# Optimization experiments

Measured on AMD Instinct MI355X. Metric: run time of the kernel, lower is better.

The kernel has to match this reference:

```python
import jax, jax.numpy as jnp
import numpy as np

H = 128          # hidden_dim
N_LAYERS = 3
N_GRAPHS = 256
LN_EPS = 1e-5


def setup_inputs() -> dict:
    key = jax.random.key(0)
    ks = jax.random.split(key, 12)
    N, E = 100000, 600000
    x = jax.random.normal(ks[0], (N, 66), dtype=jnp.float32)
    edge_index = jax.random.randint(ks[1], (2, E), 0, N, dtype=jnp.int32)
    edge_attr = jax.random.normal(ks[2], (E, 6), dtype=jnp.float32)
    batch = jnp.sort(jax.random.randint(ks[3], (N,), 0, N_GRAPHS, dtype=jnp.int32))
    # params (stored as [in, out] so y = x @ W + b)
    def lin(k, fan_in, fan_out):
        s = 1.0 / np.sqrt(fan_in)
        kw, kb = jax.random.split(k)
        return (jax.random.uniform(kw, (fan_in, fan_out), jnp.float32, -s, s),
                jax.random.uniform(kb, (fan_out,), jnp.float32, -s, s))
    w_node, b_node = lin(ks[4], 66, H)
    w_edge, b_edge = lin(ks[5], 6, H)
    mp_ws, mp_bs = [], []
    for i in range(N_LAYERS):
        w, b = lin(ks[6 + i], 3 * H, H)
        mp_ws.append(w); mp_bs.append(b)
    w_out, b_out = lin(ks[9], H, H)
    return {
        "x": x, "edge_index": edge_index, "edge_attr": edge_attr, "batch": batch,
        "w_node": w_node, "b_node": b_node, "w_edge": w_edge, "b_edge": b_edge,
        "mp_w": jnp.stack(mp_ws), "mp_b": jnp.stack(mp_bs),
        "ln_g": jnp.ones((H,), jnp.float32), "ln_b": jnp.zeros((H,), jnp.float32),
        "w_out": w_out, "b_out": b_out,
    }


def _layer_norm(h, g, b):
    mu = h.mean(-1, keepdims=True)
    var = ((h - mu) ** 2).mean(-1, keepdims=True)
    return (h - mu) * jax.lax.rsqrt(var + LN_EPS) * g + b


def reference(x, edge_index, edge_attr, batch, w_node, b_node, w_edge, b_edge,
              mp_w, mp_b, ln_g, ln_b, w_out, b_out):
    h = x @ w_node + b_node                      # [N, H]
    ef = edge_attr @ w_edge + b_edge             # [E, H]
    src, dst = edge_index[0], edge_index[1]
    for i in range(N_LAYERS):
        W = mp_w[i]                               # [3H, H], split to avoid concat
        Ws, Wd, We = W[:H], W[H:2 * H], W[2 * H:]
        # per-edge message = Linear(concat(h[src], h[dst], ef)); original takes a
        # GLOBAL mean over all edges -> single [H] vector broadcast to all nodes
        msgs = h[src] @ Ws + h[dst] @ Wd + ef @ We   # [E, H]
        mean_msg = msgs.mean(axis=0) + mp_b[i]       # [H]
        h = h + mean_msg
        h = jax.nn.relu(_layer_norm(h, ln_g, ln_b))
        # dropout is identity in eval mode
    counts = jax.ops.segment_sum(jnp.ones((h.shape[0],), h.dtype), batch,
                                 num_segments=N_GRAPHS)
    pooled = jax.ops.segment_sum(h, batch, num_segments=N_GRAPHS)
    pooled = pooled / jnp.maximum(counts, 1.0)[:, None]   # global_mean_pool
    return pooled @ w_out + b_out                 # [N_GRAPHS, H]
```

## Files before the change

### kernel.cpp

```cpp
#include <hip/hip_runtime.h>

#define HDIM 128
#define XDIM 66
#define EDIM 6
#define NGRAPHS 256
#define LN_EPS 1e-5f

#define NWORDS 25600
#define CBINS 102400
#define HB 64
#define NBX 1024
#define KP 104
#define NES 16

typedef __attribute__((ext_vector_type(8))) short sv8;
typedef __attribute__((ext_vector_type(4))) float fv4;

__device__ __forceinline__ unsigned short f2bf(float f) {
    unsigned u = __float_as_uint(f);
    return (unsigned short)((u + 0x7FFFu + ((u >> 16) & 1u)) >> 16);
}
__device__ __forceinline__ float bf2f(unsigned short u) {
    return __uint_as_float((unsigned)u << 16);
}

__global__ __launch_bounds__(1024) void k_hist(const int* __restrict__ ei,
        unsigned* __restrict__ part, int E) {
    __shared__ unsigned lh[NWORDS];
    int b = blockIdx.x;
    int s = b & (HB - 1);
    int a = b / HB;
    int t = threadIdx.x;
    for (int i = t; i < NWORDS; i += 1024) lh[i] = 0u;
    __syncthreads();
    const int* src = ei + (size_t)a * E;
    int chunk = (((E + HB - 1) / HB) + 3) & ~3;
    int lo = s * chunk;
    int hi = min(E, lo + chunk);
    if ((E & 3) == 0) {
        for (int i = lo + t * 4; i + 4 <= hi; i += 1024 * 4) {
            int4 v = *(const int4*)(src + i);
            atomicAdd(&lh[v.x >> 2], 1u << ((v.x & 3) * 8));
            atomicAdd(&lh[v.y >> 2], 1u << ((v.y & 3) * 8));
            atomicAdd(&lh[v.z >> 2], 1u << ((v.z & 3) * 8));
            atomicAdd(&lh[v.w >> 2], 1u << ((v.w & 3) * 8));
        }
    } else {
        for (int i = lo + t; i < hi; i += 1024) {
            int v = src[i];
            atomicAdd(&lh[v >> 2], 1u << ((v & 3) * 8));
        }
    }
    __syncthreads();
    unsigned* dst = part + (size_t)b * NWORDS;
    for (int i = t; i < NWORDS / 4; i += 1024)
        ((uint4*)dst)[i] = ((const uint4*)lh)[i];
}

__global__ __launch_bounds__(256) void k_hist_red(const unsigned* __restrict__ part,
        float* __restrict__ c_src, float* __restrict__ c_dst) {
    int w = blockIdx.x * 256 + threadIdx.x;
    if (w >= NWORDS) return;
    unsigned a0 = 0, a1 = 0;
    const unsigned* p0 = part + w;
    const unsigned* p1 = part + (size_t)HB * NWORDS + w;
#pragma unroll 8
    for (int s = 0; s < HB; ++s) {
        a0 += p0[(size_t)s * NWORDS];
        a1 += p1[(size_t)s * NWORDS];
    }
    float4 o0, o1;
    o0.x = (float)(a0 & 0xFF);         o0.y = (float)((a0 >> 8) & 0xFF);
    o0.z = (float)((a0 >> 16) & 0xFF); o0.w = (float)(a0 >> 24);
    o1.x = (float)(a1 & 0xFF);         o1.y = (float)((a1 >> 8) & 0xFF);
    o1.z = (float)((a1 >> 16) & 0xFF); o1.w = (float)(a1 >> 24);
    *(float4*)(c_src + 4 * w) = o0;
    *(float4*)(c_dst + 4 * w) = o1;
}

__global__ __launch_bounds__(256) void k_misc(const float* __restrict__ ea,
        float* __restrict__ sum_attr, int E, const float* __restrict__ w_node,
        unsigned short* __restrict__ wtg) {
    int b = blockIdx.x;
    int t = threadIdx.x;
    if (b < NES) {
        int nchunk = E >> 1;
        float a0 = 0, a1 = 0, a2 = 0, a3 = 0, a4 = 0, a5 = 0;
        for (int c = b * 256 + t; c < nchunk; c += NES * 256) {
            const float4* p = (const float4*)(ea + (size_t)c * 12);
            float4 v0 = p[0], v1 = p[1], v2 = p[2];
            a0 += v0.x + v1.z;  a1 += v0.y + v1.w;  a2 += v0.z + v2.x;
            a3 += v0.w + v2.y;  a4 += v1.x + v2.z;  a5 += v1.y + v2.w;
        }
#pragma unroll
        for (int m = 32; m; m >>= 1) {
            a0 += __shfl_xor(a0, m); a1 += __shfl_xor(a1, m); a2 += __shfl_xor(a2, m);
            a3 += __shfl_xor(a3, m); a4 += __shfl_xor(a4, m); a5 += __shfl_xor(a5, m);
        }
        __shared__ float sb[4][6];
        int lane = t & 63, w = t >> 6;
        if (lane == 0) {
            sb[w][0] = a0; sb[w][1] = a1; sb[w][2] = a2;
            sb[w][3] = a3; sb[w][4] = a4; sb[w][5] = a5;
        }
        __syncthreads();
        if (t < 6) {
            float s = sb[0][t] + sb[1][t] + sb[2][t] + sb[3][t];
            atomicAdd(&sum_attr[t], s);
        }
        if (b == 0 && t < 6 && (E & 1))
            atomicAdd(&sum_attr[t], ea[(size_t)(E - 1) * 6 + t]);
    } else {
        if (t < 128) {
            for (int kp = 0; kp < KP; ++kp) {
                float v = (kp < XDIM) ? w_node[kp * HDIM + t] : 0.f;
                wtg[t * KP + kp] = f2bf(v);
            }
        }
    }
}

__global__ __launch_bounds__(256) void k_xsum(const float* __restrict__ x,
        const float* __restrict__ c_src, const float* __restrict__ c_dst,
        float* __restrict__ xpart, int N) {
    int lane = threadIdx.x & 63, w = threadIdx.x >> 6;
    int wid = blockIdx.x * 4 + w, nw = gridDim.x * 4;
    float as0 = 0, ad0 = 0, as1 = 0, ad1 = 0;
    int Q = N >> 2;
    for (int q = wid; q < Q; q += nw) {
        int n = q * 4;
        const float* xr = x + (size_t)n * XDIM;
        float x0 = xr[lane];
        float x1 = xr[XDIM + lane];
        float x2 = xr[2 * XDIM + lane];
        float x3 = xr[3 * XDIM + lane];
        float4 cs = *(const float4*)(c_src + n);
        float4 cd = *(const float4*)(c_dst + n);
        as0 = fmaf(cs.x, x0, as0); as0 = fmaf(cs.y, x1, as0);
        as0 = fmaf(cs.z, x2, as0); as0 = fmaf(cs.w, x3, as0);
        ad0 = fmaf(cd.x, x0, ad0); ad0 = fmaf(cd.y, x1, ad0);
        ad0 = fmaf(cd.z, x2, ad0); ad0 = fmaf(cd.w, x3, ad0);
        if (lane < 2) {
            float e0 = xr[64 + lane];
            float e1 = xr[XDIM + 64 + lane];
            float e2 = xr[2 * XDIM + 64 + lane];
            float e3 = xr[3 * XDIM + 64 + lane];
            as1 = fmaf(cs.x, e0, as1); as1 = fmaf(cs.y, e1, as1);
            as1 = fmaf(cs.z, e2, as1); as1 = fmaf(cs.w, e3, as1);
            ad1 = fmaf(cd.x, e0, ad1); ad1 = fmaf(cd.y, e1, ad1);
            ad1 = fmaf(cd.z, e2, ad1); ad1 = fmaf(cd.w, e3, ad1);
        }
    }
    if (wid == 0) {
        for (int n = Q * 4; n < N; ++n) {
            const float* xr = x + (size_t)n * XDIM;
            float cs = c_src[n], cd = c_dst[n];
            float xv = xr[lane];
            as0 = fmaf(cs, xv, as0);
            ad0 = fmaf(cd, xv, ad0);
            if (lane < 2) {
                float xe = xr[64 + lane];
                as1 = fmaf(cs, xe, as1);
                ad1 = fmaf(cd, xe, ad1);
            }
        }
    }
    __shared__ float redS[4][XDIM], redD[4][XDIM];
    redS[w][lane] = as0;  redD[w][lane] = ad0;
    if (lane < 2) { redS[w][64 + lane] = as1;  redD[w][64 + lane] = ad1; }
    __syncthreads();
    int t = threadIdx.x;
    float* xp = xpart + (size_t)blockIdx.x * 136;
    if (t < XDIM) {
        xp[t]        = redS[0][t] + redS[1][t] + redS[2][t] + redS[3][t];
        xp[XDIM + t] = redD[0][t] + redD[1][t] + redD[2][t] + redD[3][t];
    }
}

__global__ __launch_bounds__(64) void k_xred(const float* __restrict__ xpart,
                                             float* __restrict__ xs, int nb) {
    int e = blockIdx.x;
    int lane = threadIdx.x;
    float s = 0.f;
    for (int b = lane; b < nb; b += 64)
        s += xpart[(size_t)b * 136 + e];
#pragma unroll
    for (int m = 32; m; m >>= 1) s += __shfl_xor(s, m);
    if (lane == 0) xs[e] = s;
}

__global__ __launch_bounds__(256) void k_red(const float* __restrict__ partials,
                                             float* __restrict__ sbuf, int nb) {
    int b0 = blockIdx.x * 32;
    int b1 = min(nb, b0 + 32);
    int t = threadIdx.x;
    float s0 = 0.f, s1 = 0.f;
    for (int b = b0; b < b1; ++b) {
        const float* row = partials + (size_t)b * 512;
        s0 += row[t];
        s1 += row[t + 256];
    }
    atomicAdd(&sbuf[t], s0);
    atomicAdd(&sbuf[t + 256], s1);
}

template <int FIRST>
__global__ __launch_bounds__(256) void k_mm(const float* __restrict__ sv,
        const float* __restrict__ sum_attr, const float* __restrict__ w_edge,
        const float* __restrict__ b_edge, const float* __restrict__ W,
        const float* __restrict__ mpb, float* __restrict__ mean_msg, float Ef,
        const float* __restrict__ w_node, const float* __restrict__ b_node) {
    __shared__ float sc[384];
    __shared__ float mred[256];
    int t = threadIdx.x;
    if (t < 128) {
        float ssrc, sdst;
        if (FIRST) {
            ssrc = Ef * b_node[t];
            sdst = ssrc;
#pragma unroll
            for (int k = 0; k < XDIM; ++k) {
                float wv = w_node[k * HDIM + t];
                ssrc = fmaf(sv[k], wv, ssrc);
                sdst = fmaf(sv[XDIM + k], wv, sdst);
            }
        } else {
            ssrc = sv[t] + sv[t + 128];
            sdst = sv[256 + t] + sv[384 + t];
        }
        sc[t] = ssrc;
        sc[128 + t] = sdst;
        float se = Ef * b_edge[t];
#pragma unroll
        for (int k = 0; k < EDIM; ++k) se = fmaf(sum_attr[k], w_edge[k * HDIM + t], se);
        sc[256 + t] = se;
    }
    __syncthreads();
    int col = blockIdx.x * 16 + (t & 15);
    int rg = t >> 4;
    float acc = 0.f;
#pragma unroll 4
    for (int r = rg * 24; r < rg * 24 + 24; ++r)
        acc = fmaf(sc[r], W[r * HDIM + col], acc);
    mred[t] = acc;
    __syncthreads();
    if (t < 16) {
        float s = 0.f;
#pragma unroll
        for (int g = 0; g < 16; ++g) s += mred[g * 16 + t];
        mean_msg[blockIdx.x * 16 + t] = s / Ef + mpb[blockIdx.x * 16 + t];
    }
}

__global__ __launch_bounds__(256) void k_upd0(
        const float* __restrict__ x, const unsigned short* __restrict__ wtg,
        const float* __restrict__ b_node, const float* __restrict__ mean_msg,
        const float* __restrict__ ln_g, const float* __restrict__ ln_b,
        const float* __restrict__ c_src, const float* __restrict__ c_dst,
        unsigned short* __restrict__ h, float* __restrict__ partials, int N) {
    __shared__ unsigned short xl[64 * KP];
    __shared__ unsigned short wt[128 * KP];
    int t = threadIdx.x;
    int lane = t & 63, w = t >> 6;
    {
        const uint4* srcp = (const uint4*)wtg;
        uint4* dstp = (uint4*)wt;
        for (int i = t; i < 128 * KP / 8; i += 256) dstp[i] = srcp[i];
    }
    for (int i = t; i < 64 * KP / 2; i += 256) ((unsigned*)xl)[i] = 0u;
    __syncthreads();
    int rowbase = blockIdx.x * 64;
    const float* xg = x + (size_t)rowbase * XDIM;
    int lim = min(64, N - rowbase) * XDIM;
    for (int i = t; i < 64 * XDIM; i += 256) {
        if (i < lim) {
            int r = i / XDIM, k = i - r * XDIM;
            xl[r * KP + k] = f2bf(xg[i]);
        }
    }
    int cl = lane & 15, g = lane >> 4;
    float bm[8], gg[8], lb[8];
#pragma unroll
    for (int ct = 0; ct < 8; ++ct) {
        int col = ct * 16 + cl;
        bm[ct] = b_node[col] + mean_msg[col];
        gg[ct] = ln_g[col];
        lb[ct] = ln_b[col];
    }
    __syncthreads();

    fv4 acc[8];
#pragma unroll
    for (int ct = 0; ct < 8; ++ct) acc[ct] = (fv4){0.f, 0.f, 0.f, 0.f};
#pragma unroll
    for (int ks = 0; ks < 3; ++ks) {
        sv8 a = *(const sv8*)&xl[(w * 16 + cl) * KP + ks * 32 + g * 8];
#pragma unroll
        for (int ct = 0; ct < 8; ++ct) {
            sv8 b = *(const sv8*)&wt[(ct * 16 + cl) * KP + ks * 32 + g * 8];
            acc[ct] = __builtin_amdgcn_mfma_f32_16x16x32_bf16(a, b, acc[ct], 0, 0, 0);
        }
    }
    float v[8][4];
    float s[4] = {0.f, 0.f, 0.f, 0.f};
#pragma unroll
    for (int ct = 0; ct < 8; ++ct)
#pragma unroll
        for (int e = 0; e < 4; ++e) {
            v[ct][e] = acc[ct][e] + bm[ct];
            s[e] += v[ct][e];
        }
#pragma unroll
    for (int m = 1; m < 16; m <<= 1) {
        s[0] += __shfl_xor(s[0], m); s[1] += __shfl_xor(s[1], m);
        s[2] += __shfl_xor(s[2], m); s[3] += __shfl_xor(s[3], m);
    }
    float mu[4], q[4] = {0.f, 0.f, 0.f, 0.f};
#pragma unroll
    for (int e = 0; e < 4; ++e) mu[e] = s[e] * (1.0f / HDIM);
#pragma unroll
    for (int ct = 0; ct < 8; ++ct)
#pragma unroll
        for (int e = 0; e < 4; ++e) {
            float d = v[ct][e] - mu[e];
            q[e] = fmaf(d, d, q[e]);
        }
#pragma unroll
    for (int m = 1; m < 16; m <<= 1) {
        q[0] += __shfl_xor(q[0], m); q[1] += __shfl_xor(q[1], m);
        q[2] += __shfl_xor(q[2], m); q[3] += __shfl_xor(q[3], m);
    }
    float rs[4];
#pragma unroll
    for (int e = 0; e < 4; ++e) rs[e] = rsqrtf(q[e] * (1.0f / HDIM) + LN_EPS);

    int grow = rowbase + w * 16 + g * 4;
    float4 csv = *(const float4*)(c_src + grow);
    float4 cdv = *(const float4*)(c_dst + grow);
    float cs[4] = {csv.x, csv.y, csv.z, csv.w};
    float cd[4] = {cdv.x, cdv.y, cdv.z, cdv.w};
    float accS[8], accD[8];
#pragma unroll
    for (int ct = 0; ct < 8; ++ct) { accS[ct] = 0.f; accD[ct] = 0.f; }
#pragma unroll
    for (int e = 0; e < 4; ++e) {
        int row = grow + e;
        bool ok = (row < N);
#pragma unroll
        for (int ct = 0; ct < 8; ++ct) {
            float o = fmaxf(0.f, fmaf((v[ct][e] - mu[e]) * rs[e], gg[ct], lb[ct]));
            if (ok) h[(size_t)row * HDIM + ct * 16 + cl] = f2bf(o);
            accS[ct] = fmaf(cs[e], o, accS[ct]);
            accD[ct] = fmaf(cd[e], o, accD[ct]);
        }
    }
#pragma unroll
    for (int ct = 0; ct < 8; ++ct) {
        accS[ct] += __shfl_xor(accS[ct], 16); accS[ct] += __shfl_xor(accS[ct], 32);
        accD[ct] += __shfl_xor(accD[ct], 16); accD[ct] += __shfl_xor(accD[ct], 32);
    }
    __syncthreads();
    float* redS = (float*)xl;
    float* redD = redS + 512;
    if (g == 0) {
#pragma unroll
        for (int ct = 0; ct < 8; ++ct) {
            redS[w * HDIM + ct * 16 + cl] = accS[ct];
            redD[w * HDIM + ct * 16 + cl] = accD[ct];
        }
    }
    __syncthreads();
    if (t < 128) {
        float ss = redS[t] + redS[128 + t] + redS[256 + t] + redS[384 + t];
        float dd = redD[t] + redD[128 + t] + redD[256 + t] + redD[384 + t];
        float* row = partials + (size_t)blockIdx.x * 512;
        row[t] = ss;       row[t + 128] = 0.f;
        row[t + 256] = dd; row[t + 384] = 0.f;
    }
}

__device__ __forceinline__ float4 ln_row4(const unsigned short* hp,
        float4 mm, float4 g, float4 bb) {
    ushort4 hv = *(const ushort4*)hp;
    float4 v;
    v.x = bf2f(hv.x) + mm.x; v.y = bf2f(hv.y) + mm.y;
    v.z = bf2f(hv.z) + mm.z; v.w = bf2f(hv.w) + mm.w;
    float s = v.x + v.y + v.z + v.w;
#pragma unroll
    for (int m = 1; m < 32; m <<= 1) s += __shfl_xor(s, m);
    float mu = s * (1.0f / HDIM);
    float d0 = v.x - mu, d1 = v.y - mu, d2 = v.z - mu, d3 = v.w - mu;
    float q = d0 * d0 + d1 * d1 + d2 * d2 + d3 * d3;
#pragma unroll
    for (int m = 1; m < 32; m <<= 1) q += __shfl_xor(q, m);
    float rs = rsqrtf(q * (1.0f / HDIM) + LN_EPS);
    float4 o;
    o.x = fmaxf(0.f, fmaf(d0 * rs, g.x, bb.x));
    o.y = fmaxf(0.f, fmaf(d1 * rs, g.y, bb.y));
    o.z = fmaxf(0.f, fmaf(d2 * rs, g.z, bb.z));
    o.w = fmaxf(0.f, fmaf(d3 * rs, g.w, bb.w));
    return o;
}

template <int LAST>
__global__ __launch_bounds__(256) void k_update(
        unsigned short* __restrict__ h, const float* __restrict__ mean_msg,
        const float* __restrict__ ln_g, const float* __restrict__ ln_b,
        const float* __restrict__ c_src, const float* __restrict__ c_dst,
        const int* __restrict__ batch, float* __restrict__ partials,
        float* __restrict__ pooled, int N, int cpb) {
    int t = threadIdx.x;
    int lane = t & 63, w = t >> 6;
    int half = lane >> 5, cl = lane & 31;
    int c0 = cl * 4;
    float4 mm = *(const float4*)(mean_msg + c0);
    float4 g  = *(const float4*)(ln_g + c0);
    float4 bb = *(const float4*)(ln_b + c0);
    int start = blockIdx.x * cpb;
    int end = min(N, start + cpb);
    int spw = (cpb + 3) >> 2;
    int ns = start + w * spw;
    int ne = min(end, ns + spw);
    float4 accS = {0,0,0,0}, accD = {0,0,0,0}, accP = {0,0,0,0};
    int cur_g = -1;
    int n = ns;
    for (; n + 4 <= ne; n += 4) {
        int rA = n + half, rB = n + 2 + half;
        float4 oA = ln_row4(h + (size_t)rA * HDIM + c0, mm, g, bb);
        float4 oB = ln_row4(h + (size_t)rB * HDIM + c0, mm, g, bb);
        if (LAST) {
            int gA = batch[rA], gB = batch[rB];
            if (gA != cur_g) {
                if (cur_g >= 0) {
                    atomicAdd(&pooled[cur_g * HDIM + c0],     accP.x);
                    atomicAdd(&pooled[cur_g * HDIM + c0 + 1], accP.y);
                    atomicAdd(&pooled[cur_g * HDIM + c0 + 2], accP.z);
                    atomicAdd(&pooled[cur_g * HDIM + c0 + 3], accP.w);
                }
                accP = (float4){0,0,0,0};
                cur_g = gA;
            }
            accP.x += oA.x; accP.y += oA.y; accP.z += oA.z; accP.w += oA.w;
            if (gB != cur_g) {
                if (cur_g >= 0) {
                    atomicAdd(&pooled[cur_g * HDIM + c0],     accP.x);
                    atomicAdd(&pooled[cur_g * HDIM + c0 + 1], accP.y);
                    atomicAdd(&pooled[cur_g * HDIM + c0 + 2], accP.z);
                    atomicAdd(&pooled[cur_g * HDIM + c0 + 3], accP.w);
                }
                accP = (float4){0,0,0,0};
                cur_g = gB;
            }
            accP.x += oB.x; accP.y += oB.y; accP.z += oB.z; accP.w += oB.w;
        } else {
            ushort4 pA = {f2bf(oA.x), f2bf(oA.y), f2bf(oA.z), f2bf(oA.w)};
            ushort4 pB = {f2bf(oB.x), f2bf(oB.y), f2bf(oB.z), f2bf(oB.w)};
            *(ushort4*)(h + (size_t)rA * HDIM + c0) = pA;
            *(ushort4*)(h + (size_t)rB * HDIM + c0) = pB;
            float csA = c_src[rA], cdA = c_dst[rA];
            float csB = c_src[rB], cdB = c_dst[rB];
            accS.x = fmaf(csA, oA.x, accS.x); accS.y = fmaf(csA, oA.y, accS.y);
            accS.z = fmaf(csA, oA.z, accS.z); accS.w = fmaf(csA, oA.w, accS.w);
            accS.x = fmaf(csB, oB.x, accS.x); accS.y = fmaf(csB, oB.y, accS.y);
            accS.z = fmaf(csB, oB.z, accS.z); accS.w = fmaf(csB, oB.w, accS.w);
            accD.x = fmaf(cdA, oA.x, accD.x); accD.y = fmaf(cdA, oA.y, accD.y);
            accD.z = fmaf(cdA, oA.z, accD.z); accD.w = fmaf(cdA, oA.w, accD.w);
            accD.x = fmaf(cdB, oB.x, accD.x); accD.y = fmaf(cdB, oB.y, accD.y);
            accD.z = fmaf(cdB, oB.z, accD.z); accD.w = fmaf(cdB, oB.w, accD.w);
        }
    }
    for (; n < ne; n += 2) {
        int row = n + half;
        bool ok = row < ne;
        int rsafe = ok ? row : (N - 1);
        float4 o = ln_row4(h + (size_t)rsafe * HDIM + c0, mm, g, bb);
        if (LAST) {
            if (ok) {
                int gg2 = batch[row];
                if (gg2 != cur_g) {
                    if (cur_g >= 0) {
                        atomicAdd(&pooled[cur_g * HDIM + c0],     accP.x);
                        atomicAdd(&pooled[cur_g * HDIM + c0 + 1], accP.y);
                        atomicAdd(&pooled[cur_g * HDIM + c0 + 2], accP.z);
                        atomicAdd(&pooled[cur_g * HDIM + c0 + 3], accP.w);
                    }
                    accP = (float4){0,0,0,0};
                    cur_g = gg2;
                }
                accP.x += o.x; accP.y += o.y; accP.z += o.z; accP.w += o.w;
            }
        } else if (ok) {
            ushort4 pk = {f2bf(o.x), f2bf(o.y), f2bf(o.z), f2bf(o.w)};
            *(ushort4*)(h + (size_t)row * HDIM + c0) = pk;
            float cs = c_src[row], cd = c_dst[row];
            accS.x = fmaf(cs, o.x, accS.x); accS.y = fmaf(cs, o.y, accS.y);
            accS.z = fmaf(cs, o.z, accS.z); accS.w = fmaf(cs, o.w, accS.w);
            accD.x = fmaf(cd, o.x, accD.x); accD.y = fmaf(cd, o.y, accD.y);
            accD.z = fmaf(cd, o.z, accD.z); accD.w = fmaf(cd, o.w, accD.w);
        }
    }
    if (LAST) {
        if (cur_g >= 0) {
            atomicAdd(&pooled[cur_g * HDIM + c0],     accP.x);
            atomicAdd(&pooled[cur_g * HDIM + c0 + 1], accP.y);
            atomicAdd(&pooled[cur_g * HDIM + c0 + 2], accP.z);
            atomicAdd(&pooled[cur_g * HDIM + c0 + 3], accP.w);
        }
    } else {
        __shared__ float redS[8][HDIM], redD[8][HDIM];
        int set = (w << 1) | half;
        *(float4*)(&redS[set][c0]) = accS;
        *(float4*)(&redD[set][c0]) = accD;
        __syncthreads();
        if (t < 128) {
            float ss = 0.f, dd = 0.f;
#pragma unroll
            for (int gi = 0; gi < 8; ++gi) {
                ss += redS[gi][t];
                dd += redD[gi][t];
            }
            float* row = partials + (size_t)blockIdx.x * 512;
            row[t] = ss;       row[t + 128] = 0.f;
            row[t + 256] = dd; row[t + 384] = 0.f;
        }
    }
}

__global__ __launch_bounds__(128) void k_out(const float* __restrict__ pooled,
        const int* __restrict__ batch, const float* __restrict__ w_out,
        const float* __restrict__ b_out, float* __restrict__ out, int N) {
    int gph = blockIdx.x;
    int t = threadIdx.x;
    __shared__ float p[HDIM];
    __shared__ int cntS;
    if (t == 0) {
        int lo = 0, hi = N;
        while (lo < hi) { int mid = (lo + hi) >> 1; if (batch[mid] < gph) lo = mid + 1; else hi = mid; }
        int lo2 = lo, hi2 = N;
        while (lo2 < hi2) { int mid = (lo2 + hi2) >> 1; if (batch[mid] <= gph) lo2 = mid + 1; else hi2 = mid; }
        cntS = lo2 - lo;
    }
    __syncthreads();
    float inv = 1.0f / fmaxf((float)cntS, 1.0f);
    p[t] = pooled[gph * HDIM + t] * inv;
    __syncthreads();
    float acc = b_out[t];
#pragma unroll 8
    for (int k = 0; k < HDIM; ++k) acc = fmaf(p[k], w_out[k * HDIM + t], acc);
    out[gph * HDIM + t] = acc;
}

extern "C" void kernel_launch(void* const* d_in, const int* in_sizes, int n_in,
                              void* d_out, int out_size, void* d_ws, size_t ws_size,
                              hipStream_t stream) {
    const float* x      = (const float*)d_in[0];
    const int*   ei     = (const int*)d_in[1];
    const float* ea     = (const float*)d_in[2];
    const int*   batch  = (const int*)d_in[3];
    const float* w_node = (const float*)d_in[4];
    const float* b_node = (const float*)d_in[5];
    const float* w_edge = (const float*)d_in[6];
    const float* b_edge = (const float*)d_in[7];
    const float* mp_w   = (const float*)d_in[8];
    const float* mp_b   = (const float*)d_in[9];
    const float* ln_g   = (const float*)d_in[10];
    const float* ln_b   = (const float*)d_in[11];
    const float* w_out  = (const float*)d_in[12];
    const float* b_out  = (const float*)d_in[13];
    float* out = (float*)d_out;
    int N = in_sizes[3];
    int E = in_sizes[2] / EDIM;
    float Ef = (float)E;
    int ntiles0 = (N + 63) / 64;

    float* ws = (float*)d_ws;
    size_t off = 0;
    unsigned short* h = (unsigned short*)(ws + off);
    unsigned* hist_part = (unsigned*)(ws + off);
    off += (size_t)N * HDIM / 2;
    float* partials = ws + off; off += (size_t)2048 * 512;
    float* mean_msg = ws + off; off += 128;
    float* c_src    = ws + off; off += CBINS;
    float* c_dst    = ws + off; off += CBINS;
    float* xpart    = ws + off; off += (size_t)NBX * 136;
    unsigned short* wtg = (unsigned short*)(ws + off); off += 128 * KP / 2;
    float* xs       = ws + off; off += 136;
    float* acc0     = ws + off;
    float* sum_attr = ws + off; off += 8;
    float* sbuf1    = ws + off; off += 512;
    float* sbuf2    = ws + off; off += 512;
    float* pooled   = ws + off; off += NGRAPHS * HDIM;
    size_t zero_count = (size_t)(ws + off - acc0);
    hipMemsetAsync(acc0, 0, zero_count * sizeof(float), stream);

    k_misc<<<NES + 1, 256, 0, stream>>>(ea, sum_attr, E, w_node, wtg);
    k_hist<<<2 * HB, 1024, 0, stream>>>(ei, hist_part, E);
    k_hist_red<<<(NWORDS + 255) / 256, 256, 0, stream>>>(hist_part, c_src, c_dst);
    k_xsum<<<NBX, 256, 0, stream>>>(x, c_src, c_dst, xpart, N);
    k_xred<<<2 * XDIM, 64, 0, stream>>>(xpart, xs, NBX);

    const int NB = 1024;
    int cpb = (N + NB - 1) / NB;

    k_mm<1><<<8, 256, 0, stream>>>(xs, sum_attr, w_edge, b_edge,
                                   mp_w, mp_b, mean_msg, Ef, w_node, b_node);
    k_upd0<<<ntiles0, 256, 0, stream>>>(x, wtg, b_node, mean_msg, ln_g, ln_b,
                                        c_src, c_dst, h, partials, N);
    k_red<<<(ntiles0 + 31) / 32, 256, 0, stream>>>(partials, sbuf1, ntiles0);
    k_mm<0><<<8, 256, 0, stream>>>(sbuf1, sum_attr, w_edge, b_edge,
                                   mp_w + (size_t)1 * 384 * HDIM,
                                   mp_b + (size_t)1 * HDIM, mean_msg, Ef,
                                   w_node, b_node);
    k_update<0><<<NB, 256, 0, stream>>>(h, mean_msg, ln_g, ln_b, c_src, c_dst,
                                        batch, partials, pooled, N, cpb);
    k_red<<<NB / 32, 256, 0, stream>>>(partials, sbuf2, NB);
    k_mm<0><<<8, 256, 0, stream>>>(sbuf2, sum_attr, w_edge, b_edge,
                                   mp_w + (size_t)2 * 384 * HDIM,
                                   mp_b + (size_t)2 * HDIM, mean_msg, Ef,
                                   w_node, b_node);
    k_update<1><<<NB, 256, 0, stream>>>(h, mean_msg, ln_g, ln_b, c_src, c_dst,
                                        batch, partials, pooled, N, cpb);

    k_out<<<NGRAPHS, HDIM, 0, stream>>>(pooled, batch, w_out, b_out, out, N);
}
```

Before: 169.5 us.

## Cut launches and memset by folding reductions into k_mm and merging prep kernels

Folds the edge-attr sum and weight conversion blocks into the histogram kernel, removing the separate k_misc launch. It drops k_xred and the memset by having k_mm sum the per-block partials itself and zero the pooled buffer. k_red now writes per-block partials instead of using atomics, and the xsum grid is cut from 1024 to 256 blocks. This trades a few launch and atomic costs for redundant partial reductions in each of the 8 k_mm blocks and lower xsum parallelism.

```diff
diff --git a/kernel.cpp b/kernel.cpp
--- a/kernel.cpp
+++ b/kernel.cpp
@@ -9,7 +9,7 @@
 #define NWORDS 25600
 #define CBINS 102400
 #define HB 64
-#define NBX 1024
+#define NBX 256
 #define KP 104
 #define NES 16
 
@@ -25,36 +25,76 @@
 }
 
 __global__ __launch_bounds__(1024) void k_hist(const int* __restrict__ ei,
-        unsigned* __restrict__ part, int E) {
+        unsigned* __restrict__ part, int E, const float* __restrict__ ea,
+        float* __restrict__ espart, const float* __restrict__ w_node,
+        unsigned short* __restrict__ wtg) {
     __shared__ unsigned lh[NWORDS];
     int b = blockIdx.x;
-    int s = b & (HB - 1);
-    int a = b / HB;
     int t = threadIdx.x;
-    for (int i = t; i < NWORDS; i += 1024) lh[i] = 0u;
-    __syncthreads();
-    const int* src = ei + (size_t)a * E;
-    int chunk = (((E + HB - 1) / HB) + 3) & ~3;
-    int lo = s * chunk;
-    int hi = min(E, lo + chunk);
-    if ((E & 3) == 0) {
-        for (int i = lo + t * 4; i + 4 <= hi; i += 1024 * 4) {
-            int4 v = *(const int4*)(src + i);
-            atomicAdd(&lh[v.x >> 2], 1u << ((v.x & 3) * 8));
-            atomicAdd(&lh[v.y >> 2], 1u << ((v.y & 3) * 8));
-            atomicAdd(&lh[v.z >> 2], 1u << ((v.z & 3) * 8));
-            atomicAdd(&lh[v.w >> 2], 1u << ((v.w & 3) * 8));
+    if (b < 2 * HB) {
+        int s = b & (HB - 1);
+        int a = b / HB;
+        for (int i = t; i < NWORDS; i += 1024) lh[i] = 0u;
+        __syncthreads();
+        const int* src = ei + (size_t)a * E;
+        int chunk = (((E + HB - 1) / HB) + 3) & ~3;
+        int lo = s * chunk;
+        int hi = min(E, lo + chunk);
+        if ((E & 3) == 0) {
+            for (int i = lo + t * 4; i + 4 <= hi; i += 1024 * 4) {
+                int4 v = *(const int4*)(src + i);
+                atomicAdd(&lh[v.x >> 2], 1u << ((v.x & 3) * 8));
+                atomicAdd(&lh[v.y >> 2], 1u << ((v.y & 3) * 8));
+                atomicAdd(&lh[v.z >> 2], 1u << ((v.z & 3) * 8));
+                atomicAdd(&lh[v.w >> 2], 1u << ((v.w & 3) * 8));
+            }
+        } else {
+            for (int i = lo + t; i < hi; i += 1024) {
+                int v = src[i];
+                atomicAdd(&lh[v >> 2], 1u << ((v & 3) * 8));
+            }
+        }
+        __syncthreads();
+        unsigned* dst = part + (size_t)b * NWORDS;
+        for (int i = t; i < NWORDS / 4; i += 1024)
+            ((uint4*)dst)[i] = ((const uint4*)lh)[i];
+    } else if (b < 2 * HB + NES) {
+        int b2 = b - 2 * HB;
+        int nchunk = E >> 1;
+        float a0 = 0, a1 = 0, a2 = 0, a3 = 0, a4 = 0, a5 = 0;
+        for (int c = b2 * 1024 + t; c < nchunk; c += NES * 1024) {
+            const float4* p = (const float4*)(ea + (size_t)c * 12);
+            float4 v0 = p[0], v1 = p[1], v2 = p[2];
+            a0 += v0.x + v1.z;  a1 += v0.y + v1.w;  a2 += v0.z + v2.x;
+            a3 += v0.w + v2.y;  a4 += v1.x + v2.z;  a5 += v1.y + v2.w;
+        }
+#pragma unroll
+        for (int m = 32; m; m >>= 1) {
+            a0 += __shfl_xor(a0, m); a1 += __shfl_xor(a1, m); a2 += __shfl_xor(a2, m);
+            a3 += __shfl_xor(a3, m); a4 += __shfl_xor(a4, m); a5 += __shfl_xor(a5, m);
+        }
+        float (*sb)[6] = (float(*)[6])lh;
+        int lane = t & 63, w = t >> 6;
+        if (lane == 0) {
+            sb[w][0] = a0; sb[w][1] = a1; sb[w][2] = a2;
+            sb[w][3] = a3; sb[w][4] = a4; sb[w][5] = a5;
+        }
+        __syncthreads();
+        if (t < 6) {
+            float s = 0.f;
+#pragma unroll
+            for (int wi = 0; wi < 16; ++wi) s += sb[wi][t];
+            if (b2 == 0 && (E & 1)) s += ea[(size_t)(E - 1) * 6 + t];
+            espart[b2 * 8 + t] = s;
         }
     } else {
-        for (int i = lo + t; i < hi; i += 1024) {
-            int v = src[i];
-            atomicAdd(&lh[v >> 2], 1u << ((v & 3) * 8));
-        }
-    }
-    __syncthreads();
-    unsigned* dst = part + (size_t)b * NWORDS;
-    for (int i = t; i < NWORDS / 4; i += 1024)
-        ((uint4*)dst)[i] = ((const uint4*)lh)[i];
+        if (t < 128) {
+            for (int kp = 0; kp < KP; ++kp) {
+                float v = (kp < XDIM) ? w_node[kp * HDIM + t] : 0.f;
+                wtg[t * KP + kp] = f2bf(v);
+            }
+        }
+    }
 }
 
 __global__ __launch_bounds__(256) void k_hist_red(const unsigned* __restrict__ part,
@@ -76,48 +116,6 @@
     o1.z = (float)((a1 >> 16) & 0xFF); o1.w = (float)(a1 >> 24);
     *(float4*)(c_src + 4 * w) = o0;
     *(float4*)(c_dst + 4 * w) = o1;
-}
-
-__global__ __launch_bounds__(256) void k_misc(const float* __restrict__ ea,
-        float* __restrict__ sum_attr, int E, const float* __restrict__ w_node,
-        unsigned short* __restrict__ wtg) {
-    int b = blockIdx.x;
-    int t = threadIdx.x;
-    if (b < NES) {
-        int nchunk = E >> 1;
-        float a0 = 0, a1 = 0, a2 = 0, a3 = 0, a4 = 0, a5 = 0;
-        for (int c = b * 256 + t; c < nchunk; c += NES * 256) {
-            const float4* p = (const float4*)(ea + (size_t)c * 12);
-            float4 v0 = p[0], v1 = p[1], v2 = p[2];
-            a0 += v0.x + v1.z;  a1 += v0.y + v1.w;  a2 += v0.z + v2.x;
-            a3 += v0.w + v2.y;  a4 += v1.x + v2.z;  a5 += v1.y + v2.w;
-        }
-#pragma unroll
-        for (int m = 32; m; m >>= 1) {
-            a0 += __shfl_xor(a0, m); a1 += __shfl_xor(a1, m); a2 += __shfl_xor(a2, m);
-            a3 += __shfl_xor(a3, m); a4 += __shfl_xor(a4, m); a5 += __shfl_xor(a5, m);
-        }
-        __shared__ float sb[4][6];
-        int lane = t & 63, w = t >> 6;
-        if (lane == 0) {
-            sb[w][0] = a0; sb[w][1] = a1; sb[w][2] = a2;
-            sb[w][3] = a3; sb[w][4] = a4; sb[w][5] = a5;
-        }
-        __syncthreads();
-        if (t < 6) {
-            float s = sb[0][t] + sb[1][t] + sb[2][t] + sb[3][t];
-            atomicAdd(&sum_attr[t], s);
-        }
-        if (b == 0 && t < 6 && (E & 1))
-            atomicAdd(&sum_attr[t], ea[(size_t)(E - 1) * 6 + t]);
-    } else {
-        if (t < 128) {
-            for (int kp = 0; kp < KP; ++kp) {
-                float v = (kp < XDIM) ? w_node[kp * HDIM + t] : 0.f;
-                wtg[t * KP + kp] = f2bf(v);
-            }
-        }
-    }
 }
 
 __global__ __launch_bounds__(256) void k_xsum(const float* __restrict__ x,
@@ -177,20 +175,8 @@
     }
 }
 
-__global__ __launch_bounds__(64) void k_xred(const float* __restrict__ xpart,
-                                             float* __restrict__ xs, int nb) {
-    int e = blockIdx.x;
-    int lane = threadIdx.x;
-    float s = 0.f;
-    for (int b = lane; b < nb; b += 64)
-        s += xpart[(size_t)b * 136 + e];
-#pragma unroll
-    for (int m = 32; m; m >>= 1) s += __shfl_xor(s, m);
-    if (lane == 0) xs[e] = s;
-}
-
 __global__ __launch_bounds__(256) void k_red(const float* __restrict__ partials,
-                                             float* __restrict__ sbuf, int nb) {
+                                             float* __restrict__ rpart, int nb) {
     int b0 = blockIdx.x * 32;
     int b1 = min(nb, b0 + 32);
     int t = threadIdx.x;
@@ -200,19 +186,63 @@
         s0 += row[t];
         s1 += row[t + 256];
     }
-    atomicAdd(&sbuf[t], s0);
-    atomicAdd(&sbuf[t + 256], s1);
+    rpart[(size_t)blockIdx.x * 512 + t] = s0;
+    rpart[(size_t)blockIdx.x * 512 + 256 + t] = s1;
 }
 
 template <int FIRST>
-__global__ __launch_bounds__(256) void k_mm(const float* __restrict__ sv,
-        const float* __restrict__ sum_attr, const float* __restrict__ w_edge,
+__global__ __launch_bounds__(256) void k_mm(const float* __restrict__ src, int nb,
+        const float* __restrict__ espart, const float* __restrict__ w_edge,
         const float* __restrict__ b_edge, const float* __restrict__ W,
         const float* __restrict__ mpb, float* __restrict__ mean_msg, float Ef,
-        const float* __restrict__ w_node, const float* __restrict__ b_node) {
+        const float* __restrict__ w_node, const float* __restrict__ b_node,
+        float* __restrict__ pooled) {
+    __shared__ float svl[512];
     __shared__ float sc[384];
+    __shared__ float sa[8];
     __shared__ float mred[256];
     int t = threadIdx.x;
+    {
+        float4 z = {0.f, 0.f, 0.f, 0.f};
+        for (int i = blockIdx.x * 1024 + t; i < (blockIdx.x + 1) * 1024; i += 256)
+            ((float4*)pooled)[i] = z;
+    }
+    if (t < 6) {
+        float s = 0.f;
+#pragma unroll
+        for (int b2 = 0; b2 < NES; ++b2) s += espart[b2 * 8 + t];
+        sa[t] = s;
+    }
+    if (FIRST) {
+        if (t < 136) {
+            float a0 = 0, a1 = 0, a2 = 0, a3 = 0;
+            int r = 0;
+            for (; r + 4 <= nb; r += 4) {
+                a0 += src[(size_t)r * 136 + t];
+                a1 += src[(size_t)(r + 1) * 136 + t];
+                a2 += src[(size_t)(r + 2) * 136 + t];
+                a3 += src[(size_t)(r + 3) * 136 + t];
+            }
+            for (; r < nb; ++r) a0 += src[(size_t)r * 136 + t];
+            svl[t] = a0 + a1 + a2 + a3;
+        }
+    } else {
+        float a0 = 0, a1 = 0, b0 = 0, b1 = 0;
+        int r = 0;
+        for (; r + 2 <= nb; r += 2) {
+            a0 += src[(size_t)r * 512 + t];
+            b0 += src[(size_t)r * 512 + 256 + t];
+            a1 += src[(size_t)(r + 1) * 512 + t];
+            b1 += src[(size_t)(r + 1) * 512 + 256 + t];
+        }
+        for (; r < nb; ++r) {
+            a0 += src[(size_t)r * 512 + t];
+            b0 += src[(size_t)r * 512 + 256 + t];
+        }
+        svl[t] = a0 + a1;
+        svl[256 + t] = b0 + b1;
+    }
+    __syncthreads();
     if (t < 128) {
         float ssrc, sdst;
         if (FIRST) {
@@ -221,18 +251,18 @@
 #pragma unroll
             for (int k = 0; k < XDIM; ++k) {
                 float wv = w_node[k * HDIM + t];
-                ssrc = fmaf(sv[k], wv, ssrc);
-                sdst = fmaf(sv[XDIM + k], wv, sdst);
+                ssrc = fmaf(svl[k], wv, ssrc);
+                sdst = fmaf(svl[XDIM + k], wv, sdst);
             }
         } else {
-            ssrc = sv[t] + sv[t + 128];
-            sdst = sv[256 + t] + sv[384 + t];
+            ssrc = svl[t] + svl[t + 128];
+            sdst = svl[256 + t] + svl[384 + t];
         }
         sc[t] = ssrc;
         sc[128 + t] = sdst;
         float se = Ef * b_edge[t];
 #pragma unroll
-        for (int k = 0; k < EDIM; ++k) se = fmaf(sum_attr[k], w_edge[k * HDIM + t], se);
+        for (int k = 0; k < EDIM; ++k) se = fmaf(sa[k], w_edge[k * HDIM + t], se);
         sc[256 + t] = se;
     }
     __syncthreads();
@@ -572,6 +602,10 @@
     int E = in_sizes[2] / EDIM;
     float Ef = (float)E;
     int ntiles0 = (N + 63) / 64;
+    int nrp1 = (ntiles0 + 31) / 32;
+    const int NB = 1024;
+    int nrp2 = NB / 32;
+    int cpb = (N + NB - 1) / NB;
 
     float* ws = (float*)d_ws;
     size_t off = 0;
@@ -579,45 +613,36 @@
     unsigned* hist_part = (unsigned*)(ws + off);
     off += (size_t)N * HDIM / 2;
     float* partials = ws + off; off += (size_t)2048 * 512;
+    float* rpart    = ws + off; off += (size_t)64 * 512;
     float* mean_msg = ws + off; off += 128;
     float* c_src    = ws + off; off += CBINS;
     float* c_dst    = ws + off; off += CBINS;
     float* xpart    = ws + off; off += (size_t)NBX * 136;
     unsigned short* wtg = (unsigned short*)(ws + off); off += 128 * KP / 2;
-    float* xs       = ws + off; off += 136;
-    float* acc0     = ws + off;
-    float* sum_attr = ws + off; off += 8;
-    float* sbuf1    = ws + off; off += 512;
-    float* sbuf2    = ws + off; off += 512;
+    float* espart   = ws + off; off += 128;
     float* pooled   = ws + off; off += NGRAPHS * HDIM;
-    size_t zero_count = (size_t)(ws + off - acc0);
-    hipMemsetAsync(acc0, 0, zero_count * sizeof(float), stream);
-
-    k_misc<<<NES + 1, 256, 0, stream>>>(ea, sum_attr, E, w_node, wtg);
-    k_hist<<<2 * HB, 1024, 0, stream>>>(ei, hist_part, E);
+
+    k_hist<<<2 * HB + NES + 1, 1024, 0, stream>>>(ei, hist_part, E, ea,
+                                                  espart, w_node, wtg);
     k_hist_red<<<(NWORDS + 255) / 256, 256, 0, stream>>>(hist_part, c_src, c_dst);
     k_xsum<<<NBX, 256, 0, stream>>>(x, c_src, c_dst, xpart, N);
-    k_xred<<<2 * XDIM, 64, 0, stream>>>(xpart, xs, NBX);
-
-    const int NB = 1024;
-    int cpb = (N + NB - 1) / NB;
-
-    k_mm<1><<<8, 256, 0, stream>>>(xs, sum_attr, w_edge, b_edge,
-                                   mp_w, mp_b, mean_msg, Ef, w_node, b_node);
+
+    k_mm<1><<<8, 256, 0, stream>>>(xpart, NBX, espart, w_edge, b_edge,
+                                   mp_w, mp_b, mean_msg, Ef, w_node, b_node, pooled);
     k_upd0<<<ntiles0, 256, 0, stream>>>(x, wtg, b_node, mean_msg, ln_g, ln_b,
                                         c_src, c_dst, h, partials, N);
-    k_red<<<(ntiles0 + 31) / 32, 256, 0, stream>>>(partials, sbuf1, ntiles0);
-    k_mm<0><<<8, 256, 0, stream>>>(sbuf1, sum_attr, w_edge, b_edge,
+    k_red<<<nrp1, 256, 0, stream>>>(partials, rpart, ntiles0);
+    k_mm<0><<<8, 256, 0, stream>>>(rpart, nrp1, espart, w_edge, b_edge,
                                    mp_w + (size_t)1 * 384 * HDIM,
                                    mp_b + (size_t)1 * HDIM, mean_msg, Ef,
-                                   w_node, b_node);
+                                   w_node, b_node, pooled);
     k_update<0><<<NB, 256, 0, stream>>>(h, mean_msg, ln_g, ln_b, c_src, c_dst,
                                         batch, partials, pooled, N, cpb);
-    k_red<<<NB / 32, 256, 0, stream>>>(partials, sbuf2, NB);
-    k_mm<0><<<8, 256, 0, stream>>>(sbuf2, sum_attr, w_edge, b_edge,
+    k_red<<<nrp2, 256, 0, stream>>>(partials, rpart, NB);
+    k_mm<0><<<8, 256, 0, stream>>>(rpart, nrp2, espart, w_edge, b_edge,
                                    mp_w + (size_t)2 * 384 * HDIM,
                                    mp_b + (size_t)2 * HDIM, mean_msg, Ef,
-                                   w_node, b_node);
+                                   w_node, b_node, pooled);
     k_update<1><<<NB, 256, 0, stream>>>(h, mean_msg, ln_g, ln_b, c_src, c_dst,
                                         batch, partials, pooled, N, cpb);
 
```

Measured after the change: 188.9 us. 1.11x slower.
